# Kernel optimization log

Measured on AMD Instinct MI355X. Metric: run time of the kernel, lower is better.

## Reference

```python
import jax, jax.numpy as jnp
import numpy as np

DIM = 1024
NUM_HEADS = 16
HEAD_DIM = DIM // NUM_HEADS
B, T = 2, 2048


def _rope_tables(seq_len, head_dim, dtype=jnp.float32):
    inv_freq = 1.0 / (10000.0 ** (jnp.arange(0, head_dim, 2, dtype=jnp.float32) / head_dim))
    t = jnp.arange(seq_len, dtype=jnp.float32)
    freqs = jnp.einsum('i,j->ij', t, inv_freq)            # [T, head_dim/2]
    emb = jnp.concatenate((freqs, freqs), axis=-1)         # [T, head_dim]
    return jnp.cos(emb).astype(dtype), jnp.sin(emb).astype(dtype)


def _rotate_half(x):
    x1, x2 = x[..., : x.shape[-1] // 2], x[..., x.shape[-1] // 2 :]
    return jnp.concatenate((-x2, x1), axis=-1)


def setup_inputs() -> dict:
    key = jax.random.key(0)
    ks = jax.random.split(key, 5)
    s = 1.0 / np.sqrt(DIM)
    return {
        'x': jax.random.normal(ks[0], (B, T, DIM), dtype=jnp.float32),
        'w_q': jax.random.normal(ks[1], (DIM, DIM), dtype=jnp.float32) * s,
        'w_k': jax.random.normal(ks[2], (DIM, DIM), dtype=jnp.float32) * s,
        'w_v': jax.random.normal(ks[3], (DIM, DIM), dtype=jnp.float32) * s,
        'w_out': jax.random.normal(ks[4], (DIM, DIM), dtype=jnp.float32) * s,
    }


def reference(x, w_q, w_k, w_v, w_out):
    Bn, Tn, C = x.shape
    scale = HEAD_DIM ** -0.5
    # nn.Linear(bias=False): y = x @ W^T; reshape to [B, H, T, Dh]
    def proj(w):
        y = jnp.einsum('btc,dc->btd', x, w)
        return y.reshape(Bn, Tn, NUM_HEADS, HEAD_DIM).transpose(0, 2, 1, 3)
    q, k, v = proj(w_q), proj(w_k), proj(w_v)
    cos, sin = _rope_tables(Tn, HEAD_DIM, x.dtype)         # [T, Dh], broadcasts over B,H
    q = q * cos + _rotate_half(q) * sin
    k = k * cos + _rotate_half(k) * sin
    attn = jnp.einsum('bhqd,bhkd->bhqk', q, k) * scale     # [B,H,T,T]
    attn = jax.nn.softmax(attn, axis=-1)
    out = jnp.einsum('bhqk,bhkd->bhqd', attn, v)           # [B,H,T,Dh]
    out = out.transpose(0, 2, 1, 3).reshape(Bn, Tn, C)
    return jnp.einsum('btc,dc->btd', out, w_out)
```

## Files before the change

kernel.cpp:

```cpp
#include <hip/hip_runtime.h>


typedef _Float16 f16;
typedef f16 f16x8 __attribute__((ext_vector_type(8)));
typedef __fp16 fp16x2 __attribute__((ext_vector_type(2)));
typedef float f32x4 __attribute__((ext_vector_type(4)));
typedef float f32x16 __attribute__((ext_vector_type(16)));
typedef unsigned int u32;
typedef unsigned short u16;

union V16 { uint4 u; f16x8 h; };

__device__ __forceinline__ float exp2_fast(float x) {
#if __has_builtin(__builtin_amdgcn_exp2f)
  return __builtin_amdgcn_exp2f(x);
#else
  return __expf(x * 0.69314718056f);
#endif
}

__device__ __forceinline__ u32 pkrtz(float a, float b) {
  union { fp16x2 h; u32 u; } cv;
  cv.h = __builtin_amdgcn_cvt_pkrtz(a, b);
  return cv.u;
}

#define PLSWAP(a, b)                                                          \
  asm volatile("s_nop 1\n\tv_permlane32_swap_b32 %0, %1" : "+v"(a), "+v"(b))

#define GLDS(src, dst) __builtin_amdgcn_global_load_lds(                      \
    (const __attribute__((address_space(1))) void*)(const void*)(src),        \
    (__attribute__((address_space(3))) void*)(void*)(dst), 16, 0, 0)

#define WAITBAR(N) do {                                                       \
    asm volatile("s_waitcnt vmcnt(" #N ")" ::: "memory");                     \
    __builtin_amdgcn_s_barrier();                                             \
    __builtin_amdgcn_sched_barrier(0);                                        \
  } while (0)

__global__ __launch_bounds__(256) void rope_tables_kernel(float* __restrict__ cosT,
                                                          float* __restrict__ sinT) {
  int i = blockIdx.x * 256 + threadIdx.x;
  int t = i >> 5, j = i & 31;
  float inv = 1.0f / powf(10000.0f, (float)(2 * j) * (1.0f / 64.0f));
  float ang = (float)t * inv;
  double a = (double)ang;
  cosT[i] = (float)cos(a);
  sinT[i] = (float)sin(a);
}

__global__ __launch_bounds__(256)
void cvt5_kernel(const float* __restrict__ x,  const float* __restrict__ wq,
                 const float* __restrict__ wk, const float* __restrict__ wv,
                 const float* __restrict__ wo,
                 f16* __restrict__ xh, f16* __restrict__ W3,
                 f16* __restrict__ woh) {
  int bx = blockIdx.x;
  const float* src; f16* dst; int i;
  if (bx < 4096) {
    src = x; dst = xh; i = bx * 256 + threadIdx.x;
  } else {
    int b = (bx - 4096) >> 10;
    i = ((bx - 4096) & 1023) * 256 + threadIdx.x;
    src = (b == 0) ? wq : (b == 1) ? wk : (b == 2) ? wv : wo;
    dst = (b == 3) ? woh : W3 + (size_t)b * 1048576;
  }
  float4 v = ((const float4*)src)[i];
  union { f16 h[4]; uint2 u; } cv;
  cv.h[0] = (f16)v.x; cv.h[1] = (f16)v.y; cv.h[2] = (f16)v.z; cv.h[3] = (f16)v.w;
  ((uint2*)dst)[i] = cv.u;
}

__global__ __launch_bounds__(256)
void gemm_qkv_kernel(const f16* __restrict__ X,
                     const f16* __restrict__ W3,
                     f16* __restrict__ Qo, f16* __restrict__ Ko,
                     f16* __restrict__ VTo,
                     const float* __restrict__ cosT,
                     const float* __restrict__ sinT) {
  __shared__ u16 lds[3][8192];

  const int tid = threadIdx.x, lane = tid & 63, w = tid >> 6;
  const int wr = w >> 1, wc = w & 1;
  const int c = lane & 15, g = lane >> 4;
  const int m0 = blockIdx.x * 128;
  const int by = blockIdx.y;
  const int wsel = by >> 3, hp = by & 7, h0 = hp * 2;
  const f16* Wb = W3 + (size_t)wsel * (1024 * 1024) + (size_t)hp * 128 * 1024;

  const int n1 = tid, n2 = tid + 256;
  const int r1 = n1 >> 2, gc1 = (n1 & 3) ^ ((n1 >> 3) & 3);
  const int r2 = n2 >> 2, gc2 = (n2 & 3) ^ ((n2 >> 3) & 3);
  const f16* gA1 = X + (size_t)(m0 + r1) * 1024 + gc1 * 8;
  const f16* gA2 = X + (size_t)(m0 + r2) * 1024 + gc2 * 8;
  const f16* gB1 = Wb + (size_t)r1 * 1024 + gc1 * 8;
  const f16* gB2 = Wb + (size_t)r2 * 1024 + gc2 * 8;
  const int dA1 = n1 * 8, dA2 = n2 * 8;
  const int dB1 = 4096 + n1 * 8, dB2 = 4096 + n2 * 8;

  f32x4 acc[4][4];
  const f32x4 zero = {0.f, 0.f, 0.f, 0.f};
#pragma unroll
  for (int mi = 0; mi < 4; ++mi)
#pragma unroll
    for (int ni = 0; ni < 4; ++ni) acc[mi][ni] = zero;

#define STAGE_QKV(buf, kt) do {                                               \
    const int ko = (kt) * 32;                                                 \
    GLDS(gA1 + ko, &lds[buf][dA1]);                                           \
    GLDS(gA2 + ko, &lds[buf][dA2]);                                           \
    GLDS(gB1 + ko, &lds[buf][dB1]);                                           \
    GLDS(gB2 + ko, &lds[buf][dB2]);                                           \
  } while (0)

  const int swz = (g ^ ((c >> 1) & 3)) * 8;

  STAGE_QKV(0, 0);
  STAGE_QKV(1, 1);
  WAITBAR(4);

  int cur = 0, nx2 = 2;
  for (int kt = 0; kt < 32; ++kt) {
    if (kt < 30) STAGE_QKV(nx2, kt + 2);
    V16 a[4], b[4];
#pragma unroll
    for (int mi = 0; mi < 4; ++mi)
      a[mi].u = *(const uint4*)&lds[cur][(wr * 64 + mi * 16 + c) * 32 + swz];
#pragma unroll
    for (int ni = 0; ni < 4; ++ni)
      b[ni].u = *(const uint4*)&lds[cur][4096 + (wc * 64 + ni * 16 + c) * 32 + swz];
    __builtin_amdgcn_s_setprio(1);
#pragma unroll
    for (int mi = 0; mi < 4; ++mi)
#pragma unroll
      for (int ni = 0; ni < 4; ++ni)
        acc[mi][ni] = __builtin_amdgcn_mfma_f32_16x16x32_f16(a[mi].h, b[ni].h, acc[mi][ni], 0, 0, 0);
    __builtin_amdgcn_s_setprio(0);
    if (kt < 30) WAITBAR(4); else WAITBAR(0);
    cur = (cur == 2) ? 0 : cur + 1;
    nx2 = (nx2 == 2) ? 0 : nx2 + 1;
  }

  if (wsel < 2) {
    f16* Out = (wsel == 0) ? Qo : Ko;
    const float psc = (wsel == 0) ? 0.18033688f : 1.0f;
    const int head = h0 + wc;
#pragma unroll
    for (int mi = 0; mi < 4; ++mi)
#pragma unroll
      for (int r = 0; r < 4; ++r) {
        int m = m0 + wr * 64 + mi * 16 + g * 4 + r;
        int bb = m >> 11, t = m & 2047;
        float co0 = cosT[t * 32 + c],      si0 = sinT[t * 32 + c];
        float co1 = cosT[t * 32 + 16 + c], si1 = sinT[t * 32 + 16 + c];
#pragma unroll
        for (int ni = 0; ni < 4; ++ni) {
          int d = ni * 16 + c;
          float co = (ni & 1) ? co1 : co0;
          float si = (ni & 1) ? si1 : si0;
          float partner = acc[mi][ni ^ 2][r];
          float v = (acc[mi][ni][r] * co + ((d < 32) ? -partner : partner) * si) * psc;
          Out[((size_t)(bb * 16 + head) * 2048 + t) * 64 + d] = (f16)v;
        }
      }
  } else {
    u16* sT = &lds[0][0];
    const int head = h0 + wc;
    const int bbv = m0 >> 11;
    const int t0 = (m0 & 2047) + wr * 64;
#pragma unroll
    for (int mi = 0; mi < 4; ++mi)
#pragma unroll
      for (int ni = 0; ni < 4; ++ni)
#pragma unroll
        for (int r = 0; r < 4; ++r) {
          int dl = ni * 16 + c;
          int tl = mi * 16 + g * 4 + r;
          union { f16 h; u16 u; } cv; cv.h = (f16)acc[mi][ni][r];
          sT[w * 4608 + dl * 72 + tl] = cv.u;
        }
    f16* dst = VTo + ((size_t)(bbv * 16 + head) * 64 + lane) * 2048 + t0;
    const u16* srcp = &sT[w * 4608 + lane * 72];
#pragma unroll
    for (int s = 0; s < 16; ++s)
      *(uint2*)(dst + s * 4) = *(const uint2*)(srcp + s * 4);
  }
}

__global__ __launch_bounds__(256)
void gemm_out_kernel(const f16* __restrict__ AH, const f16* __restrict__ BH,
                     float* __restrict__ outF) {
  __shared__ u16 lds[3][8192];

  const int tid = threadIdx.x, lane = tid & 63, w = tid >> 6;
  const int wr = w >> 1, wc = w & 1;
  const int c = lane & 15, g = lane >> 4;
  const int m0 = blockIdx.x * 128, n0 = blockIdx.y * 128;

  const int n1 = tid, n2 = tid + 256;
  const int r1 = n1 >> 2, gc1 = (n1 & 3) ^ ((n1 >> 3) & 3);
  const int r2 = n2 >> 2, gc2 = (n2 & 3) ^ ((n2 >> 3) & 3);
  const f16* gA1 = AH + (size_t)(m0 + r1) * 1024 + gc1 * 8;
  const f16* gA2 = AH + (size_t)(m0 + r2) * 1024 + gc2 * 8;
  const f16* gB1 = BH + (size_t)(n0 + r1) * 1024 + gc1 * 8;
  const f16* gB2 = BH + (size_t)(n0 + r2) * 1024 + gc2 * 8;
  const int dA1 = n1 * 8, dA2 = n2 * 8;
  const int dB1 = 4096 + n1 * 8, dB2 = 4096 + n2 * 8;

  f32x4 acc[4][4];
  const f32x4 zero = {0.f, 0.f, 0.f, 0.f};
#pragma unroll
  for (int mi = 0; mi < 4; ++mi)
#pragma unroll
    for (int ni = 0; ni < 4; ++ni) acc[mi][ni] = zero;

#define STAGE_OUT(buf, kt) do {                                               \
    const int ko = (kt) * 32;                                                 \
    GLDS(gA1 + ko, &lds[buf][dA1]);                                           \
    GLDS(gA2 + ko, &lds[buf][dA2]);                                           \
    GLDS(gB1 + ko, &lds[buf][dB1]);                                           \
    GLDS(gB2 + ko, &lds[buf][dB2]);                                           \
  } while (0)

  const int swz = (g ^ ((c >> 1) & 3)) * 8;

  STAGE_OUT(0, 0);
  STAGE_OUT(1, 1);
  WAITBAR(4);

  int cur = 0, nx2 = 2;
  for (int kt = 0; kt < 32; ++kt) {
    if (kt < 30) STAGE_OUT(nx2, kt + 2);
    V16 a[4], b[4];
#pragma unroll
    for (int mi = 0; mi < 4; ++mi)
      a[mi].u = *(const uint4*)&lds[cur][(wr * 64 + mi * 16 + c) * 32 + swz];
#pragma unroll
    for (int ni = 0; ni < 4; ++ni)
      b[ni].u = *(const uint4*)&lds[cur][4096 + (wc * 64 + ni * 16 + c) * 32 + swz];
    __builtin_amdgcn_s_setprio(1);
#pragma unroll
    for (int mi = 0; mi < 4; ++mi)
#pragma unroll
      for (int ni = 0; ni < 4; ++ni)
        acc[mi][ni] = __builtin_amdgcn_mfma_f32_16x16x32_f16(a[mi].h, b[ni].h, acc[mi][ni], 0, 0, 0);
    __builtin_amdgcn_s_setprio(0);
    if (kt < 30) WAITBAR(4); else WAITBAR(0);
    cur = (cur == 2) ? 0 : cur + 1;
    nx2 = (nx2 == 2) ? 0 : nx2 + 1;
  }

#pragma unroll
  for (int mi = 0; mi < 4; ++mi)
#pragma unroll
    for (int r = 0; r < 4; ++r) {
      int m = m0 + wr * 64 + mi * 16 + g * 4 + r;
#pragma unroll
      for (int ni = 0; ni < 4; ++ni)
        outF[(size_t)m * 1024 + n0 + wc * 64 + ni * 16 + c] = acc[mi][ni][r];
    }
}

__global__ __launch_bounds__(256, 2)
void attn_kernel(const f16* __restrict__ Q, const f16* __restrict__ K,
                 const f16* __restrict__ VT,
                 f16* __restrict__ OP, float* __restrict__ LP) {
  __shared__ u16 sKV[4][8192];
  __shared__ u16 sT16[4][32][36];

  const int tid = threadIdx.x, lane = tid & 63, wid = tid >> 6;
  const int q32 = lane & 31, hi = lane >> 5;
  const int bx = blockIdx.x;
  const int bh = (bx & 7) + 8 * (bx >> 7);
  const int rest = (bx >> 3) & 15;
  const int qt = rest & 7, half = rest >> 3;
  const int qbase = qt * 256 + wid * 64;
  const int t0 = half * 16;

  V16 qfa[4], qfb[4];
  const f16* qpa = Q + ((size_t)bh * 2048 + qbase + q32) * 64 + 8 * hi;
#pragma unroll
  for (int kd = 0; kd < 4; ++kd) {
    qfa[kd].u = *(const uint4*)(qpa + 16 * kd);
    qfb[kd].u = *(const uint4*)(qpa + 32 * 64 + 16 * kd);
  }

  f32x16 oa0 = 0.0f, oa1 = 0.0f, ob0 = 0.0f, ob1 = 0.0f;
  f32x16 sa0, sa1, sb0, sb1;
  float lsa = 0.f, lsb = 0.f;

  const int rr = tid >> 3;
  const int sc = ((tid & 7) ^ (rr & 7)) * 8;
  const f16* gK1 = K + ((size_t)bh * 2048 + t0 * 64 + rr) * 64 + sc;
  const f16* gK2 = gK1 + 32 * 64;
  const f16* gV1 = VT + ((size_t)bh * 64 + rr) * 2048 + t0 * 64 + sc;
  const f16* gV2 = gV1 + 32 * 2048;

#define STAGE_A(buf, j) do {                                                  \
    GLDS(gK1 + (j) * 4096, &sKV[buf][tid * 8]);                               \
    GLDS(gK2 + (j) * 4096, &sKV[buf][2048 + tid * 8]);                        \
    GLDS(gV1 + (j) * 64,   &sKV[buf][4096 + tid * 8]);                        \
    GLDS(gV2 + (j) * 64,   &sKV[buf][6144 + tid * 8]);                        \
  } while (0)

  const int swzrow = (q32 & 7) << 4;

#define QKT2(BUF) do {                                                        \
    sa0 = 0.0f; sa1 = 0.0f; sb0 = 0.0f; sb1 = 0.0f;                           \
    const char* kb_ = (const char*)&sKV[BUF][0];                              \
    __builtin_amdgcn_s_setprio(1);                                            \
    _Pragma("unroll")                                                         \
    for (int kd = 0; kd < 4; ++kd) {                                          \
      const int off = ((32 * kd + 16 * hi) ^ swzrow);                         \
      V16 kf0, kf1;                                                           \
      kf0.u = *(const uint4*)(kb_ + q32 * 128 + off);                         \
      kf1.u = *(const uint4*)(kb_ + (32 + q32) * 128 + off);                  \
      sa0 = __builtin_amdgcn_mfma_f32_32x32x16_f16(kf0.h, qfa[kd].h, sa0, 0, 0, 0);\
      sa1 = __builtin_amdgcn_mfma_f32_32x32x16_f16(kf1.h, qfa[kd].h, sa1, 0, 0, 0);\
      sb0 = __builtin_amdgcn_mfma_f32_32x32x16_f16(kf0.h, qfb[kd].h, sb0, 0, 0, 0);\
      sb1 = __builtin_amdgcn_mfma_f32_32x32x16_f16(kf1.h, qfb[kd].h, sb1, 0, 0, 0);\
    }                                                                         \
    __builtin_amdgcn_s_setprio(0);                                            \
  } while (0)

#define SMAX(S0, S1, PB, LS) do {                                             \
    u32 c0[8], c1[8];                                                         \
    _Pragma("unroll")                                                         \
    for (int m = 0; m < 8; ++m) {                                             \
      float p0 = exp2_fast(S0[2 * m]);                                        \
      float p1 = exp2_fast(S0[2 * m + 1]);                                    \
      LS += p0 + p1; c0[m] = pkrtz(p0, p1);                                   \
      float p2 = exp2_fast(S1[2 * m]);                                        \
      float p3 = exp2_fast(S1[2 * m + 1]);                                    \
      LS += p2 + p3; c1[m] = pkrtz(p2, p3);                                   \
    }                                                                         \
    { u32 y0 = c0[0], x0 = c0[2]; PLSWAP(y0, x0);                             \
      u32 y1 = c0[1], x1 = c0[3]; PLSWAP(y1, x1);                             \
      PB[0].u.x = y0; PB[0].u.y = y1; PB[0].u.z = x0; PB[0].u.w = x1;         \
      u32 y2 = c0[4], x2 = c0[6]; PLSWAP(y2, x2);                             \
      u32 y3 = c0[5], x3 = c0[7]; PLSWAP(y3, x3);                             \
      PB[1].u.x = y2; PB[1].u.y = y3; PB[1].u.z = x2; PB[1].u.w = x3;         \
      u32 y4 = c1[0], x4 = c1[2]; PLSWAP(y4, x4);                             \
      u32 y5 = c1[1], x5 = c1[3]; PLSWAP(y5, x5);                             \
      PB[2].u.x = y4; PB[2].u.y = y5; PB[2].u.z = x4; PB[2].u.w = x5;         \
      u32 y6 = c1[4], x6 = c1[6]; PLSWAP(y6, x6);                             \
      u32 y7 = c1[5], x7 = c1[7]; PLSWAP(y7, x7);                             \
      PB[3].u.x = y6; PB[3].u.y = y7; PB[3].u.z = x6; PB[3].u.w = x7; }       \
  } while (0)

#define PV2(BUF) do {                                                         \
    const char* vb_ = (const char*)&sKV[BUF][0] + 8192;                       \
    __builtin_amdgcn_s_setprio(1);                                            \
    _Pragma("unroll")                                                         \
    for (int ks = 0; ks < 4; ++ks) {                                          \
      const int off = ((32 * ks + 16 * hi) ^ swzrow);                         \
      V16 vf0, vf1;                                                           \
      vf0.u = *(const uint4*)(vb_ + q32 * 128 + off);                         \
      vf1.u = *(const uint4*)(vb_ + (32 + q32) * 128 + off);                  \
      oa0 = __builtin_amdgcn_mfma_f32_32x32x16_f16(vf0.h, pBa[ks].h, oa0, 0, 0, 0);\
      oa1 = __builtin_amdgcn_mfma_f32_32x32x16_f16(vf1.h, pBa[ks].h, oa1, 0, 0, 0);\
      ob0 = __builtin_amdgcn_mfma_f32_32x32x16_f16(vf0.h, pBb[ks].h, ob0, 0, 0, 0);\
      ob1 = __builtin_amdgcn_mfma_f32_32x32x16_f16(vf1.h, pBb[ks].h, ob1, 0, 0, 0);\
    }                                                                         \
    __builtin_amdgcn_s_setprio(0);                                            \
  } while (0)

  V16 pBa[4], pBb[4];

  STAGE_A(0, 0);
  STAGE_A(1, 1);
  WAITBAR(4);
  QKT2(0);

  for (int kt = 0; kt < 16; ++kt) {
    if (kt < 14) STAGE_A((kt + 2) & 3, kt + 2);
    SMAX(sa0, sa1, pBa, lsa);
    SMAX(sb0, sb1, pBb, lsb);
    if (kt < 14) { WAITBAR(4); } else { WAITBAR(0); }
    if (kt < 15) QKT2((kt + 1) & 3);
    PV2(kt & 3);
  }

  lsa += __shfl_xor(lsa, 32, 64);
  lsb += __shfl_xor(lsb, 32, 64);
  const size_t lbase = (size_t)(half * 32 + bh) * 2048 + qbase;
  if (hi == 0) {
    LP[lbase + q32] = lsa;
    LP[lbase + 32 + q32] = lsb;
  }

  const int qr = lane >> 1, dh = (lane & 1) * 16;
#pragma unroll
  for (int grp = 0; grp < 2; ++grp) {
#pragma unroll
    for (int dt = 0; dt < 2; ++dt) {
#pragma unroll
      for (int r = 0; r < 16; ++r) {
        float v = grp ? (dt ? ob1[r] : ob0[r]) : (dt ? oa1[r] : oa0[r]);
        union { f16 h; u16 u; } cv; cv.h = (f16)v;
        sT16[wid][q32][(r & 3) + 8 * (r >> 2) + 4 * hi] = cv.u;
      }
      __syncthreads();
      const u16* sp = &sT16[wid][qr][dh];
      uint2 a0 = *(const uint2*)(sp + 0),  a1 = *(const uint2*)(sp + 4);
      uint2 a2 = *(const uint2*)(sp + 8),  a3 = *(const uint2*)(sp + 12);
      size_t gbase = ((size_t)(half * 32 + bh) * 2048 + qbase + grp * 32 + qr) * 64
                     + 32 * dt + dh;
      *(uint2*)(OP + gbase + 0)  = a0;
      *(uint2*)(OP + gbase + 4)  = a1;
      *(uint2*)(OP + gbase + 8)  = a2;
      *(uint2*)(OP + gbase + 12) = a3;
      __syncthreads();
    }
  }
}

__global__ __launch_bounds__(256)
void merge_kernel(const f16* __restrict__ OP, const float* __restrict__ LP,
                  f16* __restrict__ OH) {
  int i = blockIdx.x * 256 + threadIdx.x;
  int d8 = i & 7, q = (i >> 3) & 2047, bh = i >> 14;
  size_t pa = ((size_t)bh * 2048 + q) * 64 + d8 * 8;
  size_t pb = pa + (size_t)32 * 2048 * 64;
  union { uint4 u; f16x8 h; } va, vb, vr;
  va.u = *(const uint4*)(OP + pa);
  vb.u = *(const uint4*)(OP + pb);
  float inv = 1.0f / (LP[bh * 2048 + q] + LP[65536 + bh * 2048 + q]);
  f16 s = (f16)inv;
  vr.h = (va.h + vb.h) * s;
  int bb = bh >> 4, hh = bh & 15;
  *(uint4*)(OH + ((size_t)bb * 2048 + q) * 1024 + hh * 64 + d8 * 8) = vr.u;
}

extern "C" void kernel_launch(void* const* d_in, const int* in_sizes, int n_in,
                              void* d_out, int out_size, void* d_ws, size_t ws_size,
                              hipStream_t stream) {
  const float* x  = (const float*)d_in[0];
  const float* wq = (const float*)d_in[1];
  const float* wk = (const float*)d_in[2];
  const float* wv = (const float*)d_in[3];
  const float* wo = (const float*)d_in[4];

  constexpr size_t SZ_X   = 4096ull * 1024 * 2;
  constexpr size_t SZ_W   = 1024ull * 1024 * 2;
  constexpr size_t SZ_QKV = 2ull * 16 * 2048 * 64 * 2;
  constexpr size_t SZ_TBL = 2048ull * 32 * 4;
  constexpr size_t SZ_OP  = 2ull * 32 * 2048 * 64 * 2;
  constexpr size_t SZ_LP  = 2ull * 32 * 2048 * 4;
  constexpr size_t NEED = SZ_X + 4 * SZ_W + 3 * SZ_QKV + 2 * SZ_TBL + SZ_OP + SZ_LP;
  if (ws_size < NEED) return;

  char* ws = (char*)d_ws;
  f16* xh  = (f16*)(ws);
  f16* W3  = (f16*)(ws + SZ_X);
  f16* woh = (f16*)(ws + SZ_X + 3 * SZ_W);
  char* p  = ws + SZ_X + 4 * SZ_W;
  f16* qb  = (f16*)(p);            p += SZ_QKV;
  f16* kb  = (f16*)(p);            p += SZ_QKV;
  f16* vT  = (f16*)(p);            p += SZ_QKV;
  float* cosT = (float*)(p);       p += SZ_TBL;
  float* sinT = (float*)(p);       p += SZ_TBL;
  f16* OPart = (f16*)(p);          p += SZ_OP;
  float* LPart = (float*)(p);
  f16* oh = xh;

  rope_tables_kernel<<<256, 256, 0, stream>>>(cosT, sinT);
  cvt5_kernel<<<8192, 256, 0, stream>>>(x, wq, wk, wv, wo, xh, W3, woh);

  gemm_qkv_kernel<<<dim3(32, 24), 256, 0, stream>>>(xh, W3, qb, kb, vT,
                                                    cosT, sinT);

  attn_kernel<<<512, 256, 0, stream>>>(qb, kb, vT, OPart, LPart);
  merge_kernel<<<2048, 256, 0, stream>>>(OPart, LPart, oh);

  gemm_out_kernel<<<dim3(32, 8), 256, 0, stream>>>(oh, woh, (float*)d_out);
}
```

Measured before the change: 123.1 us.

## Split attention KV range into three segments and run three blocks per CU

The attention kernel now splits the key/value sequence into three segments (11/11/10 tiles) instead of two and launches 768 blocks instead of 512. Shared memory drops from four KV buffers to three, and the output transpose scratch now reuses the KV buffer, which allows a launch bound of three blocks per CU. The pipeline becomes a three-buffer rotation with a full wait each iteration, and the softmax row sum uses separate partial accumulators. The merge kernel sums three partials, which adds extra partial-output traffic in exchange for better occupancy and load balance across CUs.

```diff
diff --git a/kernel.cpp b/kernel.cpp
--- a/kernel.cpp
+++ b/kernel.cpp
@@ -261,21 +261,23 @@
     }
 }
 
-__global__ __launch_bounds__(256, 2)
+__global__ __launch_bounds__(256, 3)
 void attn_kernel(const f16* __restrict__ Q, const f16* __restrict__ K,
                  const f16* __restrict__ VT,
                  f16* __restrict__ OP, float* __restrict__ LP) {
-  __shared__ u16 sKV[4][8192];
-  __shared__ u16 sT16[4][32][36];
+  __shared__ u16 sKV[3][8192];
 
   const int tid = threadIdx.x, lane = tid & 63, wid = tid >> 6;
   const int q32 = lane & 31, hi = lane >> 5;
   const int bx = blockIdx.x;
-  const int bh = (bx & 7) + 8 * (bx >> 7);
-  const int rest = (bx >> 3) & 15;
-  const int qt = rest & 7, half = rest >> 3;
+  const int r = bx >> 3;
+  const int qt = r & 7;
+  const int s2 = r >> 3;
+  const int seg = s2 % 3;
+  const int bh = (bx & 7) + 8 * (s2 / 3);
   const int qbase = qt * 256 + wid * 64;
-  const int t0 = half * 16;
+  const int tbase = seg * 11;
+  const int nt = (seg < 2) ? 11 : 10;
 
   V16 qfa[4], qfb[4];
   const f16* qpa = Q + ((size_t)bh * 2048 + qbase + q32) * 64 + 8 * hi;
@@ -291,9 +293,9 @@
 
   const int rr = tid >> 3;
   const int sc = ((tid & 7) ^ (rr & 7)) * 8;
-  const f16* gK1 = K + ((size_t)bh * 2048 + t0 * 64 + rr) * 64 + sc;
+  const f16* gK1 = K + ((size_t)bh * 2048 + tbase * 64 + rr) * 64 + sc;
   const f16* gK2 = gK1 + 32 * 64;
-  const f16* gV1 = VT + ((size_t)bh * 64 + rr) * 2048 + t0 * 64 + sc;
+  const f16* gV1 = VT + ((size_t)bh * 64 + rr) * 2048 + tbase * 64 + sc;
   const f16* gV2 = gV1 + 32 * 2048;
 
 #define STAGE_A(buf, j) do {                                                  \
@@ -325,15 +327,17 @@
 
 #define SMAX(S0, S1, PB, LS) do {                                             \
     u32 c0[8], c1[8];                                                         \
+    float ac0_ = 0.f, ac1_ = 0.f;                                             \
     _Pragma("unroll")                                                         \
     for (int m = 0; m < 8; ++m) {                                             \
       float p0 = exp2_fast(S0[2 * m]);                                        \
       float p1 = exp2_fast(S0[2 * m + 1]);                                    \
-      LS += p0 + p1; c0[m] = pkrtz(p0, p1);                                   \
+      ac0_ += p0 + p1; c0[m] = pkrtz(p0, p1);                                 \
       float p2 = exp2_fast(S1[2 * m]);                                        \
       float p3 = exp2_fast(S1[2 * m + 1]);                                    \
-      LS += p2 + p3; c1[m] = pkrtz(p2, p3);                                   \
+      ac1_ += p2 + p3; c1[m] = pkrtz(p2, p3);                                 \
     }                                                                         \
+    LS += ac0_ + ac1_;                                                        \
     { u32 y0 = c0[0], x0 = c0[2]; PLSWAP(y0, x0);                             \
       u32 y1 = c0[1], x1 = c0[3]; PLSWAP(y1, x1);                             \
       PB[0].u.x = y0; PB[0].u.y = y1; PB[0].u.z = x0; PB[0].u.w = x1;         \
@@ -372,39 +376,43 @@
   WAITBAR(4);
   QKT2(0);
 
-  for (int kt = 0; kt < 16; ++kt) {
-    if (kt < 14) STAGE_A((kt + 2) & 3, kt + 2);
+  int bw = 2, bq = 1, bp = 0;
+  for (int kt = 0; kt < nt; ++kt) {
     SMAX(sa0, sa1, pBa, lsa);
     SMAX(sb0, sb1, pBb, lsb);
-    if (kt < 14) { WAITBAR(4); } else { WAITBAR(0); }
-    if (kt < 15) QKT2((kt + 1) & 3);
-    PV2(kt & 3);
-  }
-
+    WAITBAR(0);
+    if (kt < nt - 2) STAGE_A(bw, kt + 2);
+    if (kt < nt - 1) QKT2(bq);
+    PV2(bp);
+    bp = bq; bq = bw; bw = (bw == 2) ? 0 : bw + 1;
+  }
+
+  __syncthreads();
   lsa += __shfl_xor(lsa, 32, 64);
   lsb += __shfl_xor(lsb, 32, 64);
-  const size_t lbase = (size_t)(half * 32 + bh) * 2048 + qbase;
+  const size_t lbase = (size_t)(seg * 32 + bh) * 2048 + qbase;
   if (hi == 0) {
     LP[lbase + q32] = lsa;
     LP[lbase + 32 + q32] = lsb;
   }
 
+  u16* sTT = &sKV[0][0];
   const int qr = lane >> 1, dh = (lane & 1) * 16;
 #pragma unroll
   for (int grp = 0; grp < 2; ++grp) {
 #pragma unroll
     for (int dt = 0; dt < 2; ++dt) {
 #pragma unroll
-      for (int r = 0; r < 16; ++r) {
-        float v = grp ? (dt ? ob1[r] : ob0[r]) : (dt ? oa1[r] : oa0[r]);
+      for (int r2_ = 0; r2_ < 16; ++r2_) {
+        float v = grp ? (dt ? ob1[r2_] : ob0[r2_]) : (dt ? oa1[r2_] : oa0[r2_]);
         union { f16 h; u16 u; } cv; cv.h = (f16)v;
-        sT16[wid][q32][(r & 3) + 8 * (r >> 2) + 4 * hi] = cv.u;
+        sTT[wid * 1152 + q32 * 36 + (r2_ & 3) + 8 * (r2_ >> 2) + 4 * hi] = cv.u;
       }
       __syncthreads();
-      const u16* sp = &sT16[wid][qr][dh];
+      const u16* sp = &sTT[wid * 1152 + qr * 36 + dh];
       uint2 a0 = *(const uint2*)(sp + 0),  a1 = *(const uint2*)(sp + 4);
       uint2 a2 = *(const uint2*)(sp + 8),  a3 = *(const uint2*)(sp + 12);
-      size_t gbase = ((size_t)(half * 32 + bh) * 2048 + qbase + grp * 32 + qr) * 64
+      size_t gbase = ((size_t)(seg * 32 + bh) * 2048 + qbase + grp * 32 + qr) * 64
                      + 32 * dt + dh;
       *(uint2*)(OP + gbase + 0)  = a0;
       *(uint2*)(OP + gbase + 4)  = a1;
@@ -420,14 +428,16 @@
                   f16* __restrict__ OH) {
   int i = blockIdx.x * 256 + threadIdx.x;
   int d8 = i & 7, q = (i >> 3) & 2047, bh = i >> 14;
-  size_t pa = ((size_t)bh * 2048 + q) * 64 + d8 * 8;
-  size_t pb = pa + (size_t)32 * 2048 * 64;
-  union { uint4 u; f16x8 h; } va, vb, vr;
-  va.u = *(const uint4*)(OP + pa);
-  vb.u = *(const uint4*)(OP + pb);
-  float inv = 1.0f / (LP[bh * 2048 + q] + LP[65536 + bh * 2048 + q]);
-  f16 s = (f16)inv;
-  vr.h = (va.h + vb.h) * s;
+  size_t base = ((size_t)bh * 2048 + q) * 64 + d8 * 8;
+  const size_t PSZ = (size_t)32 * 2048 * 64;
+  union { uint4 u; f16x8 h; } va, vb, vc, vr;
+  va.u = *(const uint4*)(OP + base);
+  vb.u = *(const uint4*)(OP + base + PSZ);
+  vc.u = *(const uint4*)(OP + base + 2 * PSZ);
+  float l = LP[bh * 2048 + q] + LP[65536 + bh * 2048 + q]
+          + LP[131072 + bh * 2048 + q];
+  f16 s = (f16)(1.0f / l);
+  vr.h = (va.h + vb.h + vc.h) * s;
   int bb = bh >> 4, hh = bh & 15;
   *(uint4*)(OH + ((size_t)bb * 2048 + q) * 1024 + hh * 64 + d8 * 8) = vr.u;
 }
@@ -445,8 +455,8 @@
   constexpr size_t SZ_W   = 1024ull * 1024 * 2;
   constexpr size_t SZ_QKV = 2ull * 16 * 2048 * 64 * 2;
   constexpr size_t SZ_TBL = 2048ull * 32 * 4;
-  constexpr size_t SZ_OP  = 2ull * 32 * 2048 * 64 * 2;
-  constexpr size_t SZ_LP  = 2ull * 32 * 2048 * 4;
+  constexpr size_t SZ_OP  = 3ull * 32 * 2048 * 64 * 2;
+  constexpr size_t SZ_LP  = 3ull * 32 * 2048 * 4;
   constexpr size_t NEED = SZ_X + 4 * SZ_W + 3 * SZ_QKV + 2 * SZ_TBL + SZ_OP + SZ_LP;
   if (ws_size < NEED) return;
 
@@ -470,7 +480,7 @@
   gemm_qkv_kernel<<<dim3(32, 24), 256, 0, stream>>>(xh, W3, qb, kb, vT,
                                                     cosT, sinT);
 
-  attn_kernel<<<512, 256, 0, stream>>>(qb, kb, vT, OPart, LPart);
+  attn_kernel<<<768, 256, 0, stream>>>(qb, kb, vT, OPart, LPart);
   merge_kernel<<<2048, 256, 0, stream>>>(OPart, LPart, oh);
 
   gemm_out_kernel<<<dim3(32, 8), 256, 0, stream>>>(oh, woh, (float*)d_out);
```

New measurement: 261.3 us. +112.2%, slower.
